# Performance work log

Measured on AMD Instinct MI355X. Metric: run time of the kernel, lower is better.

Reference implementation:

```python
import jax, jax.numpy as jnp
import numpy as np

H, D, HID = 32, 128, 4096
I = H * D  # inner_dim = 4096
EPS = 1e-6

def l2norm(x):
    n = jnp.sqrt(jnp.sum(x * x, axis=-1, keepdims=True))
    return x / jnp.maximum(n, EPS)

def setup_inputs() -> dict:
    key = jax.random.key(0)
    ks = jax.random.split(key, 13)
    s = 0.02
    return {
        "hidden_states": jax.random.normal(ks[0], (1, 1, HID), jnp.float32),
        "rnn_state": jax.random.normal(ks[1], (1, H, D, D), jnp.float32),
        "conv_state": jax.random.normal(ks[2], (1, 3 * I, 3), jnp.float32),
        "W_qkv": (jax.random.normal(ks[3], (3 * I, HID), jnp.float32) * s),
        "W_z": (jax.random.normal(ks[4], (I, HID), jnp.float32) * s),
        "W_a": (jax.random.normal(ks[5], (H, HID), jnp.float32) * s),
        "W_b": (jax.random.normal(ks[6], (H, HID), jnp.float32) * s),
        "conv_w": (jax.random.normal(ks[7], (3 * I, 4), jnp.float32) * 0.2),  # depthwise kernel [C,1,4] squeezed
        "conv_b": jnp.zeros((3 * I,), jnp.float32),
        "A_log": jnp.log(jax.random.uniform(ks[8], (H,), jnp.float32, 0.5, 2.0)),
        "dt_bias": (jax.random.normal(ks[9], (H,), jnp.float32) * 0.1),
        "norm_w": jnp.ones((D,), jnp.float32),
        "W_out": (jax.random.normal(ks[10], (HID, I), jnp.float32) * s),
    }

def reference(hidden_states, rnn_state, conv_state, W_qkv, W_z, W_a, W_b,
              conv_w, conv_b, A_log, dt_bias, norm_w, W_out):
    B = hidden_states.shape[0]  # == 1 (enforced by original module's view)
    # QKV projection: [B,1,3I]
    qkv = jnp.einsum('bsh,ch->bsc', hidden_states, W_qkv)
    # depthwise causal conv over window of 4 (3 cached + 1 new)
    x_in = jnp.swapaxes(qkv, 1, 2)                      # [B,3I,1]
    conv_input = jnp.concatenate([conv_state, x_in], axis=2)  # [B,3I,4]
    new_conv_state = conv_input[:, :, 1:]
    y = jnp.einsum('bck,ck->bc', conv_input, conv_w) + conv_b
    y = jax.nn.silu(y)                                  # [B,3I]
    q, k, v = jnp.split(y, 3, axis=-1)
    q = q.reshape(B, H, D); k = k.reshape(B, H, D); v = v.reshape(B, H, D)
    # gating projections
    z = jnp.einsum('bsh,ch->bsc', hidden_states, W_z)   # [B,1,I]
    beta = jax.nn.sigmoid(jnp.einsum('bsh,nh->bsn', hidden_states, W_b))[:, 0]  # [B,H]
    a = jnp.einsum('bsh,nh->bsn', hidden_states, W_a)[:, 0]                     # [B,H]
    g = -jnp.exp(A_log) * jax.nn.softplus(a + dt_bias)  # [B,H]
    qn = l2norm(q) * (1.0 / np.sqrt(D))
    kn = l2norm(k)
    # gated delta-rule state update on [B,H,D,D]
    state = rnn_state * jnp.exp(g)[:, :, None, None]
    kv_mem = jnp.einsum('bhde,bhd->bhe', state, kn)
    delta = (v - kv_mem) * beta[..., None]
    state = state + kn[..., None] * delta[:, :, None, :]
    core = jnp.einsum('bhde,bhd->bhe', state, qn)       # [B,H,D]
    # per-head RMSNorm over D (fp32)
    var = jnp.mean(core * core, axis=-1, keepdims=True)
    core = norm_w * (core * jax.lax.rsqrt(var + EPS))
    core = core.reshape(B, 1, I)
    out = jnp.einsum('bsc,hc->bsh', core * jax.nn.silu(z), W_out)
    return out, state, new_conv_state
```

## Files before the change

kernel.cpp:

```cpp
#include <hip/hip_runtime.h>
#include <math.h>

#define HID   4096
#define NH    32
#define D     128
#define I_    4096
#define QKV_ROWS 12288
#define TOTAL_ROWS 16448

#define WS_QKV   0
#define WS_Z     12288
#define WS_AB    16384
#define WS_QN    16448
#define WS_KN    20544
#define WS_V     24640
#define WS_GB    28736
#define WS_VEC   28800

__device__ __forceinline__ float wave_reduce(float x) {
    for (int off = 32; off > 0; off >>= 1) x += __shfl_down(x, off, 64);
    return x;
}

__global__ __launch_bounds__(256) void matvec_all(
    const float* __restrict__ h,
    const float* __restrict__ Wqkv, const float* __restrict__ Wz,
    const float* __restrict__ Wa,   const float* __restrict__ Wb,
    float* __restrict__ ws)
{
    const int wave = threadIdx.x >> 6;
    const int lane = threadIdx.x & 63;
    const int row  = blockIdx.x * 4 + wave;

    const float* W; float* out; int r;
    if (row < QKV_ROWS)          { W = Wqkv; r = row;             out = ws + WS_QKV; }
    else if (row < 16384)        { W = Wz;   r = row - 12288;     out = ws + WS_Z;   }
    else if (row < 16416)        { W = Wa;   r = row - 16384;     out = ws + WS_AB;  }
    else                         { W = Wb;   r = row - 16416;     out = ws + WS_AB + 32; }

    const float4* wrow = (const float4*)(W + (size_t)r * HID);
    const float4* hv   = (const float4*)h;

    float acc = 0.f;
    #pragma unroll
    for (int i = 0; i < 16; ++i) {
        float4 wv = wrow[lane + i * 64];
        float4 hh = hv[lane + i * 64];
        acc = fmaf(wv.x, hh.x, acc);
        acc = fmaf(wv.y, hh.y, acc);
        acc = fmaf(wv.z, hh.z, acc);
        acc = fmaf(wv.w, hh.w, acc);
    }
    acc = wave_reduce(acc);
    if (lane == 0) out[r] = acc;
}

__global__ __launch_bounds__(128) void head_prep(
    const float* __restrict__ ws_in,
    const float* __restrict__ conv_state,
    const float* __restrict__ conv_w,
    const float* __restrict__ conv_b,
    const float* __restrict__ A_log, const float* __restrict__ dt_bias,
    float* __restrict__ ncs_out,
    float* __restrict__ ws_out)
{
    const int hd = blockIdx.x;
    const int e  = threadIdx.x;
    const float* qkv = ws_in + WS_QKV;

    float y[3];
    #pragma unroll
    for (int j = 0; j < 3; ++j) {
        const int c = j * I_ + hd * D + e;
        const float* cs = conv_state + (size_t)c * 3;
        const float* cw = conv_w     + (size_t)c * 4;
        const float x = qkv[c];
        float val = fmaf(cs[0], cw[0], fmaf(cs[1], cw[1],
                    fmaf(cs[2], cw[2], fmaf(x, cw[3], conv_b[c]))));
        y[j] = val / (1.f + expf(-val));
        ncs_out[(size_t)c * 3 + 0] = cs[1];
        ncs_out[(size_t)c * 3 + 1] = cs[2];
        ncs_out[(size_t)c * 3 + 2] = x;
    }

    float sq = y[0] * y[0];
    float sk = y[1] * y[1];
    sq = wave_reduce(sq);
    sk = wave_reduce(sk);
    __shared__ float s_sq[2], s_sk[2];
    const int wave = threadIdx.x >> 6, lane = threadIdx.x & 63;
    if (lane == 0) { s_sq[wave] = sq; s_sk[wave] = sk; }
    __syncthreads();
    const float nq = sqrtf(s_sq[0] + s_sq[1]);
    const float nk = sqrtf(s_sk[0] + s_sk[1]);
    const float invq = (1.f / fmaxf(nq, 1e-6f)) * 0.08838834764831843f;
    const float invk =  1.f / fmaxf(nk, 1e-6f);

    ws_out[WS_QN + hd * D + e] = y[0] * invq;
    ws_out[WS_KN + hd * D + e] = y[1] * invk;
    ws_out[WS_V  + hd * D + e] = y[2];

    if (threadIdx.x == 0) {
        const float a_ = ws_in[WS_AB + hd];
        const float b_ = ws_in[WS_AB + 32 + hd];
        const float x  = a_ + dt_bias[hd];
        const float sp = fmaxf(x, 0.f) + log1pf(expf(-fabsf(x)));
        ws_out[WS_GB + hd]      = -expf(A_log[hd]) * sp;
        ws_out[WS_GB + 32 + hd] = 1.f / (1.f + expf(-b_));
    }
}

__global__ __launch_bounds__(256) void state_update(
    const float* __restrict__ rnn_state,
    const float* __restrict__ ws,
    const float* __restrict__ norm_w,
    float* __restrict__ state_out,
    float* __restrict__ vec_out)
{
    const int hd   = blockIdx.x;
    const int tid  = threadIdx.x;
    const int e    = tid & 127;
    const int half = tid >> 7;
    const int d0   = half * 64;

    const float* S  = rnn_state + (size_t)hd * D * D;
    float*       So = state_out + (size_t)hd * D * D;
    const float eg   = expf(ws[WS_GB + hd]);
    const float beta = ws[WS_GB + 32 + hd];

    __shared__ float skn[128], sqn[128];
    if (half == 0) {
        skn[e] = ws[WS_KN + hd * D + e];
        sqn[e] = ws[WS_QN + hd * D + e];
    }
    __syncthreads();

    float kv = 0.f, cq = 0.f;
    #pragma unroll 4
    for (int d = d0; d < d0 + 64; ++d) {
        const float s = S[d * D + e] * eg;
        kv = fmaf(s, skn[d], kv);
        cq = fmaf(s, sqn[d], cq);
    }
    __shared__ float pkv[2][128], pcq[2][128];
    pkv[half][e] = kv; pcq[half][e] = cq;
    __syncthreads();
    const float kvt = pkv[0][e] + pkv[1][e];
    const float cqt = pcq[0][e] + pcq[1][e];

    float kq = 0.f;
    #pragma unroll 4
    for (int d = 0; d < 128; ++d) kq = fmaf(skn[d], sqn[d], kq);

    const float delta = (ws[WS_V + hd * D + e] - kvt) * beta;
    const float core  = cqt + delta * kq;

    #pragma unroll 4
    for (int d = d0; d < d0 + 64; ++d)
        So[d * D + e] = fmaf(skn[d], delta, S[d * D + e] * eg);

    __shared__ float red[2];
    if (half == 0) {
        float c2 = wave_reduce(core * core);
        if ((tid & 63) == 0) red[tid >> 6] = c2;
    }
    __syncthreads();
    const float var = (red[0] + red[1]) * (1.f / 128.f);
    if (half == 0) {
        const float cn = norm_w[e] * core * rsqrtf(var + 1e-6f);
        const float zz = ws[WS_Z + hd * D + e];
        vec_out[hd * D + e] = cn * (zz / (1.f + expf(-zz)));
    }
}

__global__ __launch_bounds__(256) void matvec_out(
    const float* __restrict__ Wout, const float* __restrict__ vec,
    float* __restrict__ out)
{
    const int wave = threadIdx.x >> 6;
    const int lane = threadIdx.x & 63;
    const int row  = blockIdx.x * 4 + wave;

    const float4* wrow = (const float4*)(Wout + (size_t)row * I_);
    const float4* xv   = (const float4*)vec;

    float acc = 0.f;
    #pragma unroll
    for (int i = 0; i < 16; ++i) {
        float4 wv = wrow[lane + i * 64];
        float4 xx = xv[lane + i * 64];
        acc = fmaf(wv.x, xx.x, acc);
        acc = fmaf(wv.y, xx.y, acc);
        acc = fmaf(wv.z, xx.z, acc);
        acc = fmaf(wv.w, xx.w, acc);
    }
    acc = wave_reduce(acc);
    if (lane == 0) out[row] = acc;
}

extern "C" void kernel_launch(void* const* d_in, const int* in_sizes, int n_in,
                              void* d_out, int out_size, void* d_ws, size_t ws_size,
                              hipStream_t stream) {
    const float* hs         = (const float*)d_in[0];
    const float* rnn_state  = (const float*)d_in[1];
    const float* conv_state = (const float*)d_in[2];
    const float* W_qkv      = (const float*)d_in[3];
    const float* W_z        = (const float*)d_in[4];
    const float* W_a        = (const float*)d_in[5];
    const float* W_b        = (const float*)d_in[6];
    const float* conv_w     = (const float*)d_in[7];
    const float* conv_b     = (const float*)d_in[8];
    const float* A_log      = (const float*)d_in[9];
    const float* dt_bias    = (const float*)d_in[10];
    const float* norm_w     = (const float*)d_in[11];
    const float* W_out      = (const float*)d_in[12];

    float* out       = (float*)d_out;
    float* state_out = (float*)d_out + 4096;
    float* ncs_out   = (float*)d_out + 4096 + NH * D * D;
    float* ws        = (float*)d_ws;

    matvec_all<<<TOTAL_ROWS / 4, 256, 0, stream>>>(hs, W_qkv, W_z, W_a, W_b, ws);
    head_prep<<<NH, 128, 0, stream>>>(ws, conv_state, conv_w, conv_b,
                                      A_log, dt_bias, ncs_out, ws);
    state_update<<<NH, 256, 0, stream>>>(rnn_state, ws, norm_w, state_out,
                                         ws + WS_VEC);
    matvec_out<<<I_ / 4, 256, 0, stream>>>(W_out, ws + WS_VEC, out);
}
```

Baseline: 387.9 us.

## Fuse head prep and state update into one 1024-thread kernel per head

Merges the conv/normalize kernel and the delta-rule state update into a single kernel, passing q/k/v and gates through shared memory instead of the global workspace. It also widens each head's block to 1024 threads, splitting the D rows into 8 groups of 16. Each thread keeps its state slice in registers, so rnn_state is read once instead of twice. The aim is to remove one launch and the workspace round-trip and to raise parallelism in the small state-update phase; the cost is more barriers, more shared memory and only 32 large blocks.

```diff
diff --git a/kernel.cpp b/kernel.cpp
--- a/kernel.cpp
+++ b/kernel.cpp
@@ -11,11 +11,7 @@
 #define WS_QKV   0
 #define WS_Z     12288
 #define WS_AB    16384
-#define WS_QN    16448
-#define WS_KN    20544
-#define WS_V     24640
-#define WS_GB    28736
-#define WS_VEC   28800
+#define WS_VEC   16448
 
 __device__ __forceinline__ float wave_reduce(float x) {
     for (int off = 32; off > 0; off >>= 1) x += __shfl_down(x, off, 64);
@@ -55,121 +51,124 @@
     if (lane == 0) out[r] = acc;
 }
 
-__global__ __launch_bounds__(128) void head_prep(
+__global__ __launch_bounds__(1024) void head_fused(
     const float* __restrict__ ws_in,
+    const float* __restrict__ rnn_state,
     const float* __restrict__ conv_state,
     const float* __restrict__ conv_w,
     const float* __restrict__ conv_b,
     const float* __restrict__ A_log, const float* __restrict__ dt_bias,
-    float* __restrict__ ncs_out,
-    float* __restrict__ ws_out)
-{
-    const int hd = blockIdx.x;
-    const int e  = threadIdx.x;
-    const float* qkv = ws_in + WS_QKV;
-
-    float y[3];
-    #pragma unroll
-    for (int j = 0; j < 3; ++j) {
-        const int c = j * I_ + hd * D + e;
-        const float* cs = conv_state + (size_t)c * 3;
-        const float* cw = conv_w     + (size_t)c * 4;
-        const float x = qkv[c];
-        float val = fmaf(cs[0], cw[0], fmaf(cs[1], cw[1],
-                    fmaf(cs[2], cw[2], fmaf(x, cw[3], conv_b[c]))));
-        y[j] = val / (1.f + expf(-val));
-        ncs_out[(size_t)c * 3 + 0] = cs[1];
-        ncs_out[(size_t)c * 3 + 1] = cs[2];
-        ncs_out[(size_t)c * 3 + 2] = x;
-    }
-
-    float sq = y[0] * y[0];
-    float sk = y[1] * y[1];
-    sq = wave_reduce(sq);
-    sk = wave_reduce(sk);
-    __shared__ float s_sq[2], s_sk[2];
-    const int wave = threadIdx.x >> 6, lane = threadIdx.x & 63;
-    if (lane == 0) { s_sq[wave] = sq; s_sk[wave] = sk; }
-    __syncthreads();
-    const float nq = sqrtf(s_sq[0] + s_sq[1]);
-    const float nk = sqrtf(s_sk[0] + s_sk[1]);
-    const float invq = (1.f / fmaxf(nq, 1e-6f)) * 0.08838834764831843f;
-    const float invk =  1.f / fmaxf(nk, 1e-6f);
-
-    ws_out[WS_QN + hd * D + e] = y[0] * invq;
-    ws_out[WS_KN + hd * D + e] = y[1] * invk;
-    ws_out[WS_V  + hd * D + e] = y[2];
-
-    if (threadIdx.x == 0) {
-        const float a_ = ws_in[WS_AB + hd];
-        const float b_ = ws_in[WS_AB + 32 + hd];
-        const float x  = a_ + dt_bias[hd];
-        const float sp = fmaxf(x, 0.f) + log1pf(expf(-fabsf(x)));
-        ws_out[WS_GB + hd]      = -expf(A_log[hd]) * sp;
-        ws_out[WS_GB + 32 + hd] = 1.f / (1.f + expf(-b_));
-    }
-}
-
-__global__ __launch_bounds__(256) void state_update(
-    const float* __restrict__ rnn_state,
-    const float* __restrict__ ws,
     const float* __restrict__ norm_w,
     float* __restrict__ state_out,
+    float* __restrict__ ncs_out,
     float* __restrict__ vec_out)
 {
     const int hd   = blockIdx.x;
     const int tid  = threadIdx.x;
     const int e    = tid & 127;
-    const int half = tid >> 7;
-    const int d0   = half * 64;
-
-    const float* S  = rnn_state + (size_t)hd * D * D;
-    float*       So = state_out + (size_t)hd * D * D;
-    const float eg   = expf(ws[WS_GB + hd]);
-    const float beta = ws[WS_GB + 32 + hd];
-
-    __shared__ float skn[128], sqn[128];
-    if (half == 0) {
-        skn[e] = ws[WS_KN + hd * D + e];
-        sqn[e] = ws[WS_QN + hd * D + e];
-    }
-    __syncthreads();
+    const int dgrp = tid >> 7;
+    const int d0   = dgrp * 16;
+
+    __shared__ float sy[3][D];
+    __shared__ float skn[D], sqn[D];
+    __shared__ float pkv[8][D], pcq[8][D];
+    __shared__ float pkq[8];
+    __shared__ float sgb[2];
+    __shared__ float snrm[2];
+    __shared__ float sdelta[D], score[D];
+    __shared__ float red[2];
+
+    if (tid < 384) {
+        const int j  = tid >> 7;
+        const int e2 = tid & 127;
+        const int c  = j * I_ + hd * D + e2;
+        const float* cs = conv_state + (size_t)c * 3;
+        const float* cw = conv_w     + (size_t)c * 4;
+        const float x = ws_in[WS_QKV + c];
+        float val = fmaf(cs[0], cw[0], fmaf(cs[1], cw[1],
+                    fmaf(cs[2], cw[2], fmaf(x, cw[3], conv_b[c]))));
+        sy[j][e2] = val / (1.f + expf(-val));
+        ncs_out[(size_t)c * 3 + 0] = cs[1];
+        ncs_out[(size_t)c * 3 + 1] = cs[2];
+        ncs_out[(size_t)c * 3 + 2] = x;
+    }
+    if (tid == 0) {
+        const float a_ = ws_in[WS_AB + hd];
+        const float b_ = ws_in[WS_AB + 32 + hd];
+        const float x  = a_ + dt_bias[hd];
+        const float sp = fmaxf(x, 0.f) + log1pf(expf(-fabsf(x)));
+        sgb[0] = -expf(A_log[hd]) * sp;
+        sgb[1] = 1.f / (1.f + expf(-b_));
+    }
+    __syncthreads();
+
+    if (tid < 128) {
+        const int w = tid >> 6, lane = tid & 63;
+        const float v0 = sy[w][lane], v1 = sy[w][lane + 64];
+        const float ss = wave_reduce(fmaf(v0, v0, v1 * v1));
+        if (lane == 0) snrm[w] = ss;
+    }
+    __syncthreads();
+    const float invq = (1.f / fmaxf(sqrtf(snrm[0]), 1e-6f)) * 0.08838834764831843f;
+    const float invk =  1.f / fmaxf(sqrtf(snrm[1]), 1e-6f);
+    if (tid < 128) {
+        sqn[tid] = sy[0][tid] * invq;
+        skn[tid] = sy[1][tid] * invk;
+    }
+    __syncthreads();
+
+    const float eg   = expf(sgb[0]);
+    const float beta = sgb[1];
+    const float* Sp = rnn_state + (size_t)hd * D * D + (size_t)d0 * D + e;
+
+    float sreg[16];
+    #pragma unroll
+    for (int j = 0; j < 16; ++j) sreg[j] = Sp[j * D] * eg;
 
     float kv = 0.f, cq = 0.f;
-    #pragma unroll 4
-    for (int d = d0; d < d0 + 64; ++d) {
-        const float s = S[d * D + e] * eg;
-        kv = fmaf(s, skn[d], kv);
-        cq = fmaf(s, sqn[d], cq);
-    }
-    __shared__ float pkv[2][128], pcq[2][128];
-    pkv[half][e] = kv; pcq[half][e] = cq;
-    __syncthreads();
-    const float kvt = pkv[0][e] + pkv[1][e];
-    const float cqt = pcq[0][e] + pcq[1][e];
-
-    float kq = 0.f;
-    #pragma unroll 4
-    for (int d = 0; d < 128; ++d) kq = fmaf(skn[d], sqn[d], kq);
-
-    const float delta = (ws[WS_V + hd * D + e] - kvt) * beta;
-    const float core  = cqt + delta * kq;
-
-    #pragma unroll 4
-    for (int d = d0; d < d0 + 64; ++d)
-        So[d * D + e] = fmaf(skn[d], delta, S[d * D + e] * eg);
-
-    __shared__ float red[2];
-    if (half == 0) {
-        float c2 = wave_reduce(core * core);
+    #pragma unroll
+    for (int j = 0; j < 16; ++j) {
+        kv = fmaf(sreg[j], skn[d0 + j], kv);
+        cq = fmaf(sreg[j], sqn[d0 + j], cq);
+    }
+    pkv[dgrp][e] = kv;
+    pcq[dgrp][e] = cq;
+    if (e == 0) {
+        float t = 0.f;
+        #pragma unroll
+        for (int j = 0; j < 16; ++j) t = fmaf(skn[d0 + j], sqn[d0 + j], t);
+        pkq[dgrp] = t;
+    }
+    __syncthreads();
+
+    if (tid < 128) {
+        float kvt = 0.f, cqt = 0.f, kq = 0.f;
+        #pragma unroll
+        for (int g = 0; g < 8; ++g) {
+            kvt += pkv[g][tid];
+            cqt += pcq[g][tid];
+            kq  += pkq[g];
+        }
+        const float delta = (sy[2][tid] - kvt) * beta;
+        sdelta[tid] = delta;
+        const float core = fmaf(delta, kq, cqt);
+        score[tid] = core;
+        const float c2 = wave_reduce(core * core);
         if ((tid & 63) == 0) red[tid >> 6] = c2;
     }
     __syncthreads();
-    const float var = (red[0] + red[1]) * (1.f / 128.f);
-    if (half == 0) {
-        const float cn = norm_w[e] * core * rsqrtf(var + 1e-6f);
-        const float zz = ws[WS_Z + hd * D + e];
-        vec_out[hd * D + e] = cn * (zz / (1.f + expf(-zz)));
+
+    float* So = state_out + (size_t)hd * D * D + (size_t)d0 * D + e;
+    const float de = sdelta[e];
+    #pragma unroll
+    for (int j = 0; j < 16; ++j)
+        So[j * D] = fmaf(skn[d0 + j], de, sreg[j]);
+
+    if (tid < 128) {
+        const float var = (red[0] + red[1]) * (1.f / 128.f);
+        const float cn  = norm_w[tid] * score[tid] * rsqrtf(var + 1e-6f);
+        const float zz  = ws_in[WS_Z + hd * D + tid];
+        vec_out[hd * D + tid] = cn * (zz / (1.f + expf(-zz)));
     }
 }
 
@@ -221,9 +220,8 @@
     float* ws        = (float*)d_ws;
 
     matvec_all<<<TOTAL_ROWS / 4, 256, 0, stream>>>(hs, W_qkv, W_z, W_a, W_b, ws);
-    head_prep<<<NH, 128, 0, stream>>>(ws, conv_state, conv_w, conv_b,
-                                      A_log, dt_bias, ncs_out, ws);
-    state_update<<<NH, 256, 0, stream>>>(rnn_state, ws, norm_w, state_out,
-                                         ws + WS_VEC);
+    head_fused<<<NH, 1024, 0, stream>>>(ws, rnn_state, conv_state, conv_w, conv_b,
+                                        A_log, dt_bias, norm_w,
+                                        state_out, ncs_out, ws + WS_VEC);
     matvec_out<<<I_ / 4, 256, 0, stream>>>(W_out, ws + WS_VEC, out);
 }
```

Measured after the change: 375.9 us. 1.03x faster.
